# Optimization experiments

Measured on AMD Instinct MI355X. Metric: run time of the kernel, lower is better.

The kernel has to match this reference:

```python
import jax, jax.numpy as jnp
import numpy as np

NUM_TOKENS = 5000

def setup_inputs() -> dict:
    key = jax.random.key(0)
    # x: [N, T, F] indices in [0, NUM_TOKENS)
    x = jax.random.randint(key, (32, 512, 10), 0, NUM_TOKENS, dtype=jnp.int64 if jax.config.jax_enable_x64 else jnp.int32)
    return {"x": x}

def reference(x) -> jnp.ndarray:
    # Multi-hot encode: out[n, t, x[n, t, f]] = 1 for all f.
    # Duplicate indices just re-set to 1 (matches original semantics).
    N, T, F = x.shape
    n_idx = jnp.arange(N)[:, None, None]  # broadcast over T, F
    t_idx = jnp.arange(T)[None, :, None]  # broadcast over N, F
    out = jnp.zeros((N, T, NUM_TOKENS), dtype=jnp.float32)
    return out.at[n_idx, t_idx, x].set(1.0)
```

## Files before the change

kernel.cpp:

```cpp
#include <hip/hip_runtime.h>


#define NUM_TOKENS 5000
#define NFEAT 10
#define NCHUNK (NUM_TOKENS / 4)

typedef float vfloat4 __attribute__((ext_vector_type(4)));

__global__ __launch_bounds__(256) void tenhot_kernel(const int* __restrict__ x,
                                                     float* __restrict__ out) {
    __shared__ vfloat4 row_lds[NCHUNK];

    const int row = blockIdx.x;
    const int tid = threadIdx.x;

    const vfloat4 z = {0.f, 0.f, 0.f, 0.f};
#pragma unroll
    for (int i = tid; i < NCHUNK; i += 256) {
        row_lds[i] = z;
    }

    __syncthreads();

    if (tid < NFEAT) {
        const int idx = x[row * NFEAT + tid];
        reinterpret_cast<float*>(row_lds)[idx] = 1.0f;
    }

    __syncthreads();

    vfloat4* __restrict__ row4 =
        reinterpret_cast<vfloat4*>(out + (size_t)row * NUM_TOKENS);
#pragma unroll
    for (int i = tid; i < NCHUNK; i += 256) {
        __builtin_nontemporal_store(row_lds[i], &row4[i]);
    }
}

extern "C" void kernel_launch(void* const* d_in, const int* in_sizes, int n_in,
                              void* d_out, int out_size, void* d_ws, size_t ws_size,
                              hipStream_t stream) {
    const int* x = (const int*)d_in[0];
    float* out = (float*)d_out;
    const int n_rows = in_sizes[0] / NFEAT;
    tenhot_kernel<<<n_rows, 256, 0, stream>>>(x, out);
}
```

Measured before the change: 330.2 us.

## Split multi-hot into grid-stride zero fill and separate scatter kernel

Replaces the per-row kernel, which staged each row in LDS and then stored it, with two launches. A grid-stride kernel zeroes the whole output with nontemporal vector stores, and a second kernel scatters the 1.0 values directly into global memory. This removes the LDS staging and the barriers, at the cost of a second launch and a dependency between the two kernels. The scatter writes land on lines that were just streamed out as nontemporal stores, so they may need extra memory traffic.

```diff
diff --git a/kernel.cpp b/kernel.cpp
--- a/kernel.cpp
+++ b/kernel.cpp
@@ -3,37 +3,27 @@
 
 #define NUM_TOKENS 5000
 #define NFEAT 10
-#define NCHUNK (NUM_TOKENS / 4)
 
 typedef float vfloat4 __attribute__((ext_vector_type(4)));
 
-__global__ __launch_bounds__(256) void tenhot_kernel(const int* __restrict__ x,
-                                                     float* __restrict__ out) {
-    __shared__ vfloat4 row_lds[NCHUNK];
+__global__ __launch_bounds__(256) void zero_kernel(float* __restrict__ out,
+                                                   int nchunks) {
+    vfloat4* __restrict__ o4 = reinterpret_cast<vfloat4*>(out);
+    const vfloat4 z = {0.f, 0.f, 0.f, 0.f};
+    const int stride = gridDim.x * blockDim.x;
+    for (int i = blockIdx.x * blockDim.x + threadIdx.x; i < nchunks; i += stride) {
+        __builtin_nontemporal_store(z, &o4[i]);
+    }
+}
 
-    const int row = blockIdx.x;
-    const int tid = threadIdx.x;
-
-    const vfloat4 z = {0.f, 0.f, 0.f, 0.f};
-#pragma unroll
-    for (int i = tid; i < NCHUNK; i += 256) {
-        row_lds[i] = z;
-    }
-
-    __syncthreads();
-
-    if (tid < NFEAT) {
-        const int idx = x[row * NFEAT + tid];
-        reinterpret_cast<float*>(row_lds)[idx] = 1.0f;
-    }
-
-    __syncthreads();
-
-    vfloat4* __restrict__ row4 =
-        reinterpret_cast<vfloat4*>(out + (size_t)row * NUM_TOKENS);
-#pragma unroll
-    for (int i = tid; i < NCHUNK; i += 256) {
-        __builtin_nontemporal_store(row_lds[i], &row4[i]);
+__global__ __launch_bounds__(256) void scatter_kernel(const int* __restrict__ x,
+                                                      float* __restrict__ out,
+                                                      int n) {
+    const int i = blockIdx.x * blockDim.x + threadIdx.x;
+    if (i < n) {
+        const int idx = x[i];
+        const int row = i / NFEAT;
+        out[(size_t)row * NUM_TOKENS + idx] = 1.0f;
     }
 }
 
@@ -42,6 +32,11 @@
                               hipStream_t stream) {
     const int* x = (const int*)d_in[0];
     float* out = (float*)d_out;
-    const int n_rows = in_sizes[0] / NFEAT;
-    tenhot_kernel<<<n_rows, 256, 0, stream>>>(x, out);
+    const int n_idx = in_sizes[0];
+    const int n_rows = n_idx / NFEAT;
+    const int nchunks = n_rows * (NUM_TOKENS / 4);
+
+    zero_kernel<<<2048, 256, 0, stream>>>(out, nchunks);
+
+    scatter_kernel<<<(n_idx + 255) / 256, 256, 0, stream>>>(x, out, n_idx);
 }
```

Result: slower. 366.4 us (+11.0%).

## Zero output directly in global memory and scatter ones, eight rows per block

Applied to the files above, without the earlier changes.

Removes the LDS staging buffer. Each block now zeroes eight output rows directly in global memory with vector stores, synchronizes, then scatters the 1.0 values for its 80 indices straight into global memory. This drops the shared-memory round trip and the per-row block overhead, and gives each block more work. In exchange it switches from nontemporal to regular stores. It also relies on the block barrier to order the zeroing stores before the scatter stores, and assumes the row count is a multiple of eight.

```diff
diff --git a/kernel.cpp b/kernel.cpp
--- a/kernel.cpp
+++ b/kernel.cpp
@@ -3,37 +3,32 @@
 
 #define NUM_TOKENS 5000
 #define NFEAT 10
-#define NCHUNK (NUM_TOKENS / 4)
+#define ROWS_PER_BLOCK 8
+#define IDX_PER_BLOCK (ROWS_PER_BLOCK * NFEAT)
+#define CHUNKS_PER_BLOCK (ROWS_PER_BLOCK * NUM_TOKENS / 4)
 
 typedef float vfloat4 __attribute__((ext_vector_type(4)));
 
-__global__ __launch_bounds__(256) void tenhot_kernel(const int* __restrict__ x,
-                                                     float* __restrict__ out) {
-    __shared__ vfloat4 row_lds[NCHUNK];
-
-    const int row = blockIdx.x;
+__global__ __launch_bounds__(256) void tenhot_fused(const int* __restrict__ x,
+                                                    float* __restrict__ out) {
+    const int b = blockIdx.x;
     const int tid = threadIdx.x;
 
+    float* __restrict__ base = out + (size_t)b * (ROWS_PER_BLOCK * NUM_TOKENS);
+    vfloat4* __restrict__ base4 = reinterpret_cast<vfloat4*>(base);
+
     const vfloat4 z = {0.f, 0.f, 0.f, 0.f};
-#pragma unroll
-    for (int i = tid; i < NCHUNK; i += 256) {
-        row_lds[i] = z;
+#pragma unroll 4
+    for (int i = tid; i < CHUNKS_PER_BLOCK; i += 256) {
+        base4[i] = z;
     }
 
     __syncthreads();
 
-    if (tid < NFEAT) {
-        const int idx = x[row * NFEAT + tid];
-        reinterpret_cast<float*>(row_lds)[idx] = 1.0f;
-    }
-
-    __syncthreads();
-
-    vfloat4* __restrict__ row4 =
-        reinterpret_cast<vfloat4*>(out + (size_t)row * NUM_TOKENS);
-#pragma unroll
-    for (int i = tid; i < NCHUNK; i += 256) {
-        __builtin_nontemporal_store(row_lds[i], &row4[i]);
+    if (tid < IDX_PER_BLOCK) {
+        const int idx = x[b * IDX_PER_BLOCK + tid];
+        const int r = tid / NFEAT;
+        base[r * NUM_TOKENS + idx] = 1.0f;
     }
 }
 
@@ -43,5 +38,6 @@
     const int* x = (const int*)d_in[0];
     float* out = (float*)d_out;
     const int n_rows = in_sizes[0] / NFEAT;
-    tenhot_kernel<<<n_rows, 256, 0, stream>>>(x, out);
+    const int n_blocks = n_rows / ROWS_PER_BLOCK;
+    tenhot_fused<<<n_blocks, 256, 0, stream>>>(x, out);
 }
```

After: 340.3 us. 3.1% more time.
